# Optimization experiments

Hardware: AMD Instinct MI355X
Metric: run time of the kernel (lower is better)

## Reference

```python
import jax, jax.numpy as jnp
import numpy as np

HIGH_DENSITY = 1000.0
GRID = 128          # W = D = H
NUM_COLORS = 6
N_POINTS = 4194304  # ~2^22 query samples
EXPECTED_DENSITY_SCALE = 1.0
TEMPERATURE = 1.0
HALF_EXTENT = GRID / 2.0  # voxel_size 1.0, grid centered at origin -> AABB [-64, 64]


def trilinear_sample(vol, pts):
    """torch grid_sample(mode='bilinear', align_corners=False, padding='zeros') on a 3D grid.
    vol: [X, Y, Z, C]; pts: [N, 3] normalized (x, y, z) in [-1, 1]. Returns [N, C]."""
    X, Y, Z, C = vol.shape
    sizes = jnp.array([X, Y, Z], dtype=pts.dtype)
    pos = ((pts + 1.0) * sizes - 1.0) * 0.5  # align_corners=False unnormalize
    base = jnp.floor(pos)
    frac = pos - base                         # [N, 3]
    base = base.astype(jnp.int32)
    maxi = jnp.array([X - 1, Y - 1, Z - 1], dtype=jnp.int32)
    out = jnp.zeros((pts.shape[0], C), dtype=vol.dtype)
    for dx in (0, 1):
        for dy in (0, 1):
            for dz in (0, 1):
                off = jnp.array([dx, dy, dz], dtype=jnp.int32)
                idx = base + off
                valid = jnp.all((idx >= 0) & (idx <= maxi), axis=-1)  # zero padding
                ic = jnp.clip(idx, 0, maxi)
                v = vol[ic[:, 0], ic[:, 1], ic[:, 2]]                 # [N, C] gather
                offf = jnp.array([dx, dy, dz], dtype=pts.dtype)
                w = jnp.prod(jnp.where(offf == 1.0, frac, 1.0 - frac), axis=-1)
                out = out + v * (w * valid.astype(pts.dtype))[:, None]
    return out


def st_softmax(x, temperature):
    """Straight-through softmax: hard one-hot(argmax) forward, softmax(x*T) gradient."""
    soft = jax.nn.softmax(x * temperature, axis=-1)
    hard = jax.nn.one_hot(jnp.argmax(x, axis=-1), x.shape[-1], dtype=x.dtype)
    return soft + jax.lax.stop_gradient(hard - soft)


def setup_inputs() -> dict:
    key = jax.random.key(0)
    k1, k2, k3, k4 = jax.random.split(key, 4)
    points = jax.random.uniform(k1, (N_POINTS, 3), dtype=jnp.float32,
                                minval=-60.0, maxval=60.0)
    densities = jax.random.normal(k2, (GRID, GRID, GRID, 2), dtype=jnp.float32)
    features = jax.random.normal(k3, (GRID, GRID, GRID, NUM_COLORS), dtype=jnp.float32)
    palette = jax.random.uniform(k4, (NUM_COLORS, 3), dtype=jnp.float32)
    return {"points": points, "densities": densities, "features": features,
            "palette": palette}


def reference(points, densities, features, palette):
    # normalize world points from AABB to [-1, 1] (adjust_dynamic_range, slack=True)
    npts = points / HALF_EXTENT                           # [N, 3]
    # density pre-activation: abs(raw * expected_density_scale)
    dens_pre = jnp.abs(densities * EXPECTED_DENSITY_SCALE)  # [X, Y, Z, 2]
    d_interp = trilinear_sample(dens_pre, npts)           # [N, 2]
    f_interp = trilinear_sample(features, npts)           # [N, NUM_COLORS]
    # VA quantization: ST softmax over {empty, occupied} logits -> hard occupancy
    d_soft = st_softmax(d_interp, TEMPERATURE)            # [N, 2]
    density = d_soft[:, 1:2] * HIGH_DENSITY               # [N, 1]
    # ST softmax over palette weights -> hard palette color lookup
    f_soft = st_softmax(f_interp, TEMPERATURE)            # [N, NUM_COLORS]
    rgb = f_soft @ palette                                # [N, 3]
    return jnp.concatenate([density, rgb], axis=-1)       # [N, 4]
```

## Files before the change

### kernel.cpp

```cpp
#include <hip/hip_runtime.h>

static constexpr int G = 128;
static constexpr size_t NVOX = (size_t)G * G * G;
static constexpr size_t ENTRIES_PER_PAR = (size_t)64 * 64 * 64;
static constexpr size_t NENTRIES = 8 * ENTRIES_PER_PAR;
static constexpr size_t P_BYTES = NENTRIES * 64;
static constexpr size_t C_BYTES = NVOX * 8;
static constexpr size_t WS_TWOSTAGE = P_BYTES + C_BYTES;
static constexpr size_t WS_DIRECT   = P_BYTES;


__device__ __forceinline__ uint32_t quant8(float v) {
    float c = fminf(fmaxf(v, -4.0f), 4.0f);
    return (uint32_t)((c + 4.0f) * 31.875f + 0.5f);
}

__device__ __forceinline__ uint2 make_rec8(const float2* __restrict__ dens,
                                           const float* __restrict__ feat,
                                           int vox) {
    float2 d = dens[vox];
    float delta = fabsf(d.y) - fabsf(d.x);
    int code = (int)((delta + 8.0f) * 4095.9375f + 0.5f);
    code = code < 0 ? 0 : (code > 65535 ? 65535 : code);
    const float2* fp = (const float2*)(feat + (size_t)vox * 6);
    float2 a = fp[0], b = fp[1], c = fp[2];
    uint2 r;
    r.x = (uint32_t)code | (quant8(a.x) << 16) | (quant8(a.y) << 24);
    r.y = quant8(b.x) | (quant8(b.y) << 8) | (quant8(c.x) << 16) | (quant8(c.y) << 24);
    return r;
}

__global__ __launch_bounds__(256) void compress_voxels(const float2* __restrict__ dens,
                                                       const float* __restrict__ feat,
                                                       uint2* __restrict__ C) {
    size_t v = (size_t)blockIdx.x * blockDim.x + threadIdx.x;
    if (v >= NVOX) return;
    C[v] = make_rec8(dens, feat, (int)v);
}

__global__ __launch_bounds__(256) void build_blocks_compact(const uint2* __restrict__ C,
                                                            uint4* __restrict__ P4) {
    size_t t = (size_t)blockIdx.x * blockDim.x + threadIdx.x;
    if (t >= NENTRIES) return;
    int p = (int)(t >> 18);
    int e = (int)(t & (ENTRIES_PER_PAR - 1));
    int xb = e >> 12, yb = (e >> 6) & 63, zb = e & 63;
    int x0 = 2 * xb + ((p >> 2) & 1);
    int y0 = 2 * yb + ((p >> 1) & 1);
    int z0 = 2 * zb + (p & 1);

    uint2 r[8];
    #pragma unroll
    for (int s = 0; s < 8; ++s) {
        int x = x0 + ((s >> 2) & 1); x = x < G ? x : G - 1;
        int y = y0 + ((s >> 1) & 1); y = y < G ? y : G - 1;
        int z = z0 + (s & 1);        z = z < G ? z : G - 1;
        r[s] = C[(size_t)(x * G + y) * G + z];
    }
    size_t o = t * 4;
    P4[o + 0] = make_uint4(r[0].x, r[0].y, r[1].x, r[1].y);
    P4[o + 1] = make_uint4(r[2].x, r[2].y, r[3].x, r[3].y);
    P4[o + 2] = make_uint4(r[4].x, r[4].y, r[5].x, r[5].y);
    P4[o + 3] = make_uint4(r[6].x, r[6].y, r[7].x, r[7].y);
}

__global__ __launch_bounds__(256) void build_blocks_direct(const float2* __restrict__ dens,
                                                           const float* __restrict__ feat,
                                                           uint4* __restrict__ P4) {
    size_t t = (size_t)blockIdx.x * blockDim.x + threadIdx.x;
    if (t >= NENTRIES) return;
    int p = (int)(t >> 18);
    int e = (int)(t & (ENTRIES_PER_PAR - 1));
    int xb = e >> 12, yb = (e >> 6) & 63, zb = e & 63;
    int x0 = 2 * xb + ((p >> 2) & 1);
    int y0 = 2 * yb + ((p >> 1) & 1);
    int z0 = 2 * zb + (p & 1);

    uint2 r[8];
    #pragma unroll
    for (int s = 0; s < 8; ++s) {
        int x = x0 + ((s >> 2) & 1); x = x < G ? x : G - 1;
        int y = y0 + ((s >> 1) & 1); y = y < G ? y : G - 1;
        int z = z0 + (s & 1);        z = z < G ? z : G - 1;
        r[s] = make_rec8(dens, feat, (x * G + y) * G + z);
    }
    size_t o = t * 4;
    P4[o + 0] = make_uint4(r[0].x, r[0].y, r[1].x, r[1].y);
    P4[o + 1] = make_uint4(r[2].x, r[2].y, r[3].x, r[3].y);
    P4[o + 2] = make_uint4(r[4].x, r[4].y, r[5].x, r[5].y);
    P4[o + 3] = make_uint4(r[6].x, r[6].y, r[7].x, r[7].y);
}

__global__ __launch_bounds__(256) void voxel_main(
    const float* __restrict__ points,
    const uint4* __restrict__ P4,
    const float2* __restrict__ dens,
    const float* __restrict__ palette,
    float4* __restrict__ out, int n)
{
#pragma clang fp contract(off)
    int i = blockIdx.x * blockDim.x + threadIdx.x;
    if (i >= n) return;

    float px_ = points[3 * i + 0];
    float py_ = points[3 * i + 1];
    float pz_ = points[3 * i + 2];

    float posx = ((px_ / 64.0f + 1.0f) * 128.0f - 1.0f) * 0.5f;
    float posy = ((py_ / 64.0f + 1.0f) * 128.0f - 1.0f) * 0.5f;
    float posz = ((pz_ / 64.0f + 1.0f) * 128.0f - 1.0f) * 0.5f;

    float bx = floorf(posx), by = floorf(posy), bz = floorf(posz);
    int ix = (int)bx, iy = (int)by, iz = (int)bz;
    float fx = posx - bx, fy = posy - by, fz = posz - bz;

    float wx0 = 1.0f - fx, wx1 = fx;
    float wy0 = 1.0f - fy, wy1 = fy;
    float wz0 = 1.0f - fz, wz1 = fz;

    float w[8];
    w[0] = (wx0 * wy0) * wz0; w[1] = (wx0 * wy0) * wz1;
    w[2] = (wx0 * wy1) * wz0; w[3] = (wx0 * wy1) * wz1;
    w[4] = (wx1 * wy0) * wz0; w[5] = (wx1 * wy0) * wz1;
    w[6] = (wx1 * wy1) * wz0; w[7] = (wx1 * wy1) * wz1;

    int p = ((ix & 1) << 2) | ((iy & 1) << 1) | (iz & 1);
    int e = ((ix >> 1) << 12) | ((iy >> 1) << 6) | (iz >> 1);
    const uint4* L = P4 + (((size_t)p << 18) + (size_t)e) * 4;
    uint4 L0 = L[0], L1 = L[1], L2 = L[2], L3 = L[3];

    float S = 0.0f;
    float F0 = 0.f, F1 = 0.f, F2 = 0.f, F3 = 0.f, F4 = 0.f, F5 = 0.f;
    bool suspect = false;

    uint32_t wl[8] = {L0.x, L0.z, L1.x, L1.z, L2.x, L2.z, L3.x, L3.z};
    uint32_t wh[8] = {L0.y, L0.w, L1.y, L1.w, L2.y, L2.w, L3.y, L3.w};

    #pragma unroll
    for (int s = 0; s < 8; ++s) {
        uint32_t lo = wl[s], hi = wh[s];
        uint32_t code = lo & 0xffffu;
        suspect = suspect || (code == 0u) || (code == 65535u);
        float dl = (float)code * (16.0f / 65535.0f) - 8.0f;
        float ws = w[s];
        S  += dl * ws;
        F0 += (float)((lo >> 16) & 255u) * ws;
        F1 += (float)(lo >> 24) * ws;
        F2 += (float)(hi & 255u) * ws;
        F3 += (float)((hi >> 8) & 255u) * ws;
        F4 += (float)((hi >> 16) & 255u) * ws;
        F5 += (float)(hi >> 24) * ws;
    }

    float density;
    if (!suspect && fabsf(S) > 4e-4f) {
        density = (S > 0.0f) ? 1000.0f : 0.0f;
    } else {
        double D0 = 0.0, D1 = 0.0;
        #pragma unroll
        for (int s = 0; s < 8; ++s) {
            int idx = ((ix + ((s >> 2) & 1)) * G + (iy + ((s >> 1) & 1))) * G + (iz + (s & 1));
            float2 dv = dens[idx];
            D0 += fabs((double)dv.x) * (double)w[s];
            D1 += fabs((double)dv.y) * (double)w[s];
        }
        density = (D1 > D0) ? 1000.0f : 0.0f;
    }

    int k = 0;
    float m = F0;
    if (F1 > m) { m = F1; k = 1; }
    if (F2 > m) { m = F2; k = 2; }
    if (F3 > m) { m = F3; k = 3; }
    if (F4 > m) { m = F4; k = 4; }
    if (F5 > m) { m = F5; k = 5; }

    float4 o;
    o.x = density;
    o.y = palette[3 * k + 0];
    o.z = palette[3 * k + 1];
    o.w = palette[3 * k + 2];
    out[i] = o;
}

__global__ __launch_bounds__(256) void voxel_art_direct(
    const float* __restrict__ points,
    const float2* __restrict__ dens,
    const float* __restrict__ feat,
    const float* __restrict__ palette,
    float4* __restrict__ out, int n)
{
#pragma clang fp contract(off)
    int i = blockIdx.x * blockDim.x + threadIdx.x;
    if (i >= n) return;
    float px = points[3 * i], py = points[3 * i + 1], pz = points[3 * i + 2];
    float posx = ((px / 64.0f + 1.0f) * 128.0f - 1.0f) * 0.5f;
    float posy = ((py / 64.0f + 1.0f) * 128.0f - 1.0f) * 0.5f;
    float posz = ((pz / 64.0f + 1.0f) * 128.0f - 1.0f) * 0.5f;
    float bx = floorf(posx), by = floorf(posy), bz = floorf(posz);
    int ix = (int)bx, iy = (int)by, iz = (int)bz;
    float fx = posx - bx, fy = posy - by, fz = posz - bz;
    int basei = (ix * G + iy) * G + iz;
    float wx[2] = {1.0f - fx, fx}, wy[2] = {1.0f - fy, fy}, wz[2] = {1.0f - fz, fz};
    double d0 = 0.0, d1 = 0.0;
    float f0 = 0, f1 = 0, f2 = 0, f3 = 0, f4 = 0, f5 = 0;
    #pragma unroll
    for (int dx = 0; dx < 2; ++dx)
    #pragma unroll
    for (int dy = 0; dy < 2; ++dy)
    #pragma unroll
    for (int dz = 0; dz < 2; ++dz) {
        int idx = basei + dx * (G * G) + dy * G + dz;
        float wq = (wx[dx] * wy[dy]) * wz[dz];
        float2 dv = dens[idx];
        d0 += fabs((double)dv.x) * (double)wq;
        d1 += fabs((double)dv.y) * (double)wq;
        const float2* fp2 = (const float2*)(feat + (size_t)idx * 6);
        float2 a = fp2[0], b = fp2[1], c = fp2[2];
        f0 += a.x * wq; f1 += a.y * wq; f2 += b.x * wq;
        f3 += b.y * wq; f4 += c.x * wq; f5 += c.y * wq;
    }
    float density = (d1 > d0) ? 1000.0f : 0.0f;
    int k = 0; float m = f0;
    if (f1 > m) { m = f1; k = 1; }
    if (f2 > m) { m = f2; k = 2; }
    if (f3 > m) { m = f3; k = 3; }
    if (f4 > m) { m = f4; k = 4; }
    if (f5 > m) { m = f5; k = 5; }
    out[i] = make_float4(density, palette[3 * k], palette[3 * k + 1], palette[3 * k + 2]);
}

extern "C" void kernel_launch(void* const* d_in, const int* in_sizes, int n_in,
                              void* d_out, int out_size, void* d_ws, size_t ws_size,
                              hipStream_t stream) {
    const float*  points  = (const float*)d_in[0];
    const float2* dens    = (const float2*)d_in[1];
    const float*  feat    = (const float*)d_in[2];
    const float*  palette = (const float*)d_in[3];
    float4*       out     = (float4*)d_out;

    int n = in_sizes[0] / 3;
    int threads = 256;
    int blocks = (n + threads - 1) / threads;

    if (ws_size >= WS_TWOSTAGE) {
        uint4* P4 = (uint4*)d_ws;
        uint2* C  = (uint2*)((char*)d_ws + P_BYTES);
        compress_voxels<<<(int)((NVOX + 255) / 256), 256, 0, stream>>>(dens, feat, C);
        build_blocks_compact<<<(int)((NENTRIES + 255) / 256), 256, 0, stream>>>(C, P4);
        voxel_main<<<blocks, threads, 0, stream>>>(points, P4, dens, palette, out, n);
    } else if (ws_size >= WS_DIRECT) {
        uint4* P4 = (uint4*)d_ws;
        build_blocks_direct<<<(int)((NENTRIES + 255) / 256), 256, 0, stream>>>(dens, feat, P4);
        voxel_main<<<blocks, threads, 0, stream>>>(points, P4, dens, palette, out, n);
    } else {
        voxel_art_direct<<<blocks, threads, 0, stream>>>(points, dens, feat, palette, out, n);
    }
}
```

Before: 269.3 us.

## Build all parity blocks per entry from shared neighbourhood; process two points per thread

The block-building kernel now has each thread load a 3x3x3 neighbourhood of compressed voxels once and emit all eight parity-shifted 2x2x2 records, instead of one thread per parity re-reading eight voxels. The main lookup kernel handles two points per thread, loading coordinates with float2 loads and issuing both points' table gathers before the decode math to raise memory-level parallelism. This costs more registers per thread and fewer threads in flight.

```diff
diff --git a/kernel.cpp b/kernel.cpp
--- a/kernel.cpp
+++ b/kernel.cpp
@@ -38,30 +38,45 @@
     C[v] = make_rec8(dens, feat, (int)v);
 }
 
-__global__ __launch_bounds__(256) void build_blocks_compact(const uint2* __restrict__ C,
-                                                            uint4* __restrict__ P4) {
+__global__ __launch_bounds__(256) void build_blocks_v2(const uint2* __restrict__ C,
+                                                       uint4* __restrict__ P4) {
     size_t t = (size_t)blockIdx.x * blockDim.x + threadIdx.x;
-    if (t >= NENTRIES) return;
-    int p = (int)(t >> 18);
-    int e = (int)(t & (ENTRIES_PER_PAR - 1));
-    int xb = e >> 12, yb = (e >> 6) & 63, zb = e & 63;
-    int x0 = 2 * xb + ((p >> 2) & 1);
-    int y0 = 2 * yb + ((p >> 1) & 1);
-    int z0 = 2 * zb + (p & 1);
-
-    uint2 r[8];
-    #pragma unroll
-    for (int s = 0; s < 8; ++s) {
-        int x = x0 + ((s >> 2) & 1); x = x < G ? x : G - 1;
-        int y = y0 + ((s >> 1) & 1); y = y < G ? y : G - 1;
-        int z = z0 + (s & 1);        z = z < G ? z : G - 1;
-        r[s] = C[(size_t)(x * G + y) * G + z];
-    }
-    size_t o = t * 4;
-    P4[o + 0] = make_uint4(r[0].x, r[0].y, r[1].x, r[1].y);
-    P4[o + 1] = make_uint4(r[2].x, r[2].y, r[3].x, r[3].y);
-    P4[o + 2] = make_uint4(r[4].x, r[4].y, r[5].x, r[5].y);
-    P4[o + 3] = make_uint4(r[6].x, r[6].y, r[7].x, r[7].y);
+    if (t >= ENTRIES_PER_PAR) return;
+    int xb = (int)(t >> 12), yb = (int)((t >> 6) & 63), zb = (int)(t & 63);
+
+    int xs[3], ys[3], zs[3];
+    #pragma unroll
+    for (int d = 0; d < 3; ++d) {
+        int x = 2 * xb + d; xs[d] = x < G ? x : G - 1;
+        int y = 2 * yb + d; ys[d] = y < G ? y : G - 1;
+        int z = 2 * zb + d; zs[d] = z < G ? z : G - 1;
+    }
+
+    uint2 r[3][3][3];
+    #pragma unroll
+    for (int dx = 0; dx < 3; ++dx)
+        #pragma unroll
+        for (int dy = 0; dy < 3; ++dy) {
+            const uint2* row = C + (size_t)(xs[dx] * G + ys[dy]) * G;
+            #pragma unroll
+            for (int dz = 0; dz < 3; ++dz)
+                r[dx][dy][dz] = row[zs[dz]];
+        }
+
+    size_t e4 = t * 4;
+    #pragma unroll
+    for (int p = 0; p < 8; ++p) {
+        int px = (p >> 2) & 1, py = (p >> 1) & 1, pz = p & 1;
+        uint4* dst = P4 + ((size_t)p << 20) + e4;
+        uint2 s0 = r[px + 0][py + 0][pz + 0], s1 = r[px + 0][py + 0][pz + 1];
+        uint2 s2 = r[px + 0][py + 1][pz + 0], s3 = r[px + 0][py + 1][pz + 1];
+        uint2 s4 = r[px + 1][py + 0][pz + 0], s5 = r[px + 1][py + 0][pz + 1];
+        uint2 s6 = r[px + 1][py + 1][pz + 0], s7 = r[px + 1][py + 1][pz + 1];
+        dst[0] = make_uint4(s0.x, s0.y, s1.x, s1.y);
+        dst[1] = make_uint4(s2.x, s2.y, s3.x, s3.y);
+        dst[2] = make_uint4(s4.x, s4.y, s5.x, s5.y);
+        dst[3] = make_uint4(s6.x, s6.y, s7.x, s7.y);
+    }
 }
 
 __global__ __launch_bounds__(256) void build_blocks_direct(const float2* __restrict__ dens,
@@ -75,7 +90,6 @@
     int x0 = 2 * xb + ((p >> 2) & 1);
     int y0 = 2 * yb + ((p >> 1) & 1);
     int z0 = 2 * zb + (p & 1);
-
     uint2 r[8];
     #pragma unroll
     for (int s = 0; s < 8; ++s) {
@@ -91,7 +105,81 @@
     P4[o + 3] = make_uint4(r[6].x, r[6].y, r[7].x, r[7].y);
 }
 
-__global__ __launch_bounds__(256) void voxel_main(
+struct PtWork {
+    int ix, iy, iz;
+    float w[8];
+    const uint4* L;
+};
+
+__device__ __forceinline__ void pt_setup(float px_, float py_, float pz_,
+                                         const uint4* __restrict__ P4, PtWork& W) {
+    float posx = ((px_ / 64.0f + 1.0f) * 128.0f - 1.0f) * 0.5f;
+    float posy = ((py_ / 64.0f + 1.0f) * 128.0f - 1.0f) * 0.5f;
+    float posz = ((pz_ / 64.0f + 1.0f) * 128.0f - 1.0f) * 0.5f;
+    float bx = floorf(posx), by = floorf(posy), bz = floorf(posz);
+    W.ix = (int)bx; W.iy = (int)by; W.iz = (int)bz;
+    float fx = posx - bx, fy = posy - by, fz = posz - bz;
+    float wx0 = 1.0f - fx, wx1 = fx;
+    float wy0 = 1.0f - fy, wy1 = fy;
+    float wz0 = 1.0f - fz, wz1 = fz;
+    W.w[0] = (wx0 * wy0) * wz0; W.w[1] = (wx0 * wy0) * wz1;
+    W.w[2] = (wx0 * wy1) * wz0; W.w[3] = (wx0 * wy1) * wz1;
+    W.w[4] = (wx1 * wy0) * wz0; W.w[5] = (wx1 * wy0) * wz1;
+    W.w[6] = (wx1 * wy1) * wz0; W.w[7] = (wx1 * wy1) * wz1;
+    int p = ((W.ix & 1) << 2) | ((W.iy & 1) << 1) | (W.iz & 1);
+    int e = ((W.ix >> 1) << 12) | ((W.iy >> 1) << 6) | (W.iz >> 1);
+    W.L = P4 + (((size_t)p << 18) + (size_t)e) * 4;
+}
+
+__device__ __forceinline__ float4 pt_finish(const PtWork& W,
+                                            uint4 L0, uint4 L1, uint4 L2, uint4 L3,
+                                            const float2* __restrict__ dens,
+                                            const float* __restrict__ palette) {
+    float S = 0.0f;
+    float F0 = 0.f, F1 = 0.f, F2 = 0.f, F3 = 0.f, F4 = 0.f, F5 = 0.f;
+    bool suspect = false;
+    uint32_t wl[8] = {L0.x, L0.z, L1.x, L1.z, L2.x, L2.z, L3.x, L3.z};
+    uint32_t wh[8] = {L0.y, L0.w, L1.y, L1.w, L2.y, L2.w, L3.y, L3.w};
+    #pragma unroll
+    for (int s = 0; s < 8; ++s) {
+        uint32_t lo = wl[s], hi = wh[s];
+        uint32_t code = lo & 0xffffu;
+        suspect = suspect || (code == 0u) || (code == 65535u);
+        float dl = (float)code * (16.0f / 65535.0f) - 8.0f;
+        float ws = W.w[s];
+        S  += dl * ws;
+        F0 += (float)((lo >> 16) & 255u) * ws;
+        F1 += (float)(lo >> 24) * ws;
+        F2 += (float)(hi & 255u) * ws;
+        F3 += (float)((hi >> 8) & 255u) * ws;
+        F4 += (float)((hi >> 16) & 255u) * ws;
+        F5 += (float)(hi >> 24) * ws;
+    }
+    float density;
+    if (!suspect && fabsf(S) > 4e-4f) {
+        density = (S > 0.0f) ? 1000.0f : 0.0f;
+    } else {
+        double D0 = 0.0, D1 = 0.0;
+        #pragma unroll
+        for (int s = 0; s < 8; ++s) {
+            int idx = ((W.ix + ((s >> 2) & 1)) * G + (W.iy + ((s >> 1) & 1))) * G + (W.iz + (s & 1));
+            float2 dv = dens[idx];
+            D0 += fabs((double)dv.x) * (double)W.w[s];
+            D1 += fabs((double)dv.y) * (double)W.w[s];
+        }
+        density = (D1 > D0) ? 1000.0f : 0.0f;
+    }
+    int k = 0;
+    float m = F0;
+    if (F1 > m) { m = F1; k = 1; }
+    if (F2 > m) { m = F2; k = 2; }
+    if (F3 > m) { m = F3; k = 3; }
+    if (F4 > m) { m = F4; k = 4; }
+    if (F5 > m) { m = F5; k = 5; }
+    return make_float4(density, palette[3 * k], palette[3 * k + 1], palette[3 * k + 2]);
+}
+
+__global__ __launch_bounds__(256) void voxel_main2(
     const float* __restrict__ points,
     const uint4* __restrict__ P4,
     const float2* __restrict__ dens,
@@ -99,88 +187,26 @@
     float4* __restrict__ out, int n)
 {
 #pragma clang fp contract(off)
-    int i = blockIdx.x * blockDim.x + threadIdx.x;
-    if (i >= n) return;
-
-    float px_ = points[3 * i + 0];
-    float py_ = points[3 * i + 1];
-    float pz_ = points[3 * i + 2];
-
-    float posx = ((px_ / 64.0f + 1.0f) * 128.0f - 1.0f) * 0.5f;
-    float posy = ((py_ / 64.0f + 1.0f) * 128.0f - 1.0f) * 0.5f;
-    float posz = ((pz_ / 64.0f + 1.0f) * 128.0f - 1.0f) * 0.5f;
-
-    float bx = floorf(posx), by = floorf(posy), bz = floorf(posz);
-    int ix = (int)bx, iy = (int)by, iz = (int)bz;
-    float fx = posx - bx, fy = posy - by, fz = posz - bz;
-
-    float wx0 = 1.0f - fx, wx1 = fx;
-    float wy0 = 1.0f - fy, wy1 = fy;
-    float wz0 = 1.0f - fz, wz1 = fz;
-
-    float w[8];
-    w[0] = (wx0 * wy0) * wz0; w[1] = (wx0 * wy0) * wz1;
-    w[2] = (wx0 * wy1) * wz0; w[3] = (wx0 * wy1) * wz1;
-    w[4] = (wx1 * wy0) * wz0; w[5] = (wx1 * wy0) * wz1;
-    w[6] = (wx1 * wy1) * wz0; w[7] = (wx1 * wy1) * wz1;
-
-    int p = ((ix & 1) << 2) | ((iy & 1) << 1) | (iz & 1);
-    int e = ((ix >> 1) << 12) | ((iy >> 1) << 6) | (iz >> 1);
-    const uint4* L = P4 + (((size_t)p << 18) + (size_t)e) * 4;
-    uint4 L0 = L[0], L1 = L[1], L2 = L[2], L3 = L[3];
-
-    float S = 0.0f;
-    float F0 = 0.f, F1 = 0.f, F2 = 0.f, F3 = 0.f, F4 = 0.f, F5 = 0.f;
-    bool suspect = false;
-
-    uint32_t wl[8] = {L0.x, L0.z, L1.x, L1.z, L2.x, L2.z, L3.x, L3.z};
-    uint32_t wh[8] = {L0.y, L0.w, L1.y, L1.w, L2.y, L2.w, L3.y, L3.w};
-
-    #pragma unroll
-    for (int s = 0; s < 8; ++s) {
-        uint32_t lo = wl[s], hi = wh[s];
-        uint32_t code = lo & 0xffffu;
-        suspect = suspect || (code == 0u) || (code == 65535u);
-        float dl = (float)code * (16.0f / 65535.0f) - 8.0f;
-        float ws = w[s];
-        S  += dl * ws;
-        F0 += (float)((lo >> 16) & 255u) * ws;
-        F1 += (float)(lo >> 24) * ws;
-        F2 += (float)(hi & 255u) * ws;
-        F3 += (float)((hi >> 8) & 255u) * ws;
-        F4 += (float)((hi >> 16) & 255u) * ws;
-        F5 += (float)(hi >> 24) * ws;
-    }
-
-    float density;
-    if (!suspect && fabsf(S) > 4e-4f) {
-        density = (S > 0.0f) ? 1000.0f : 0.0f;
-    } else {
-        double D0 = 0.0, D1 = 0.0;
-        #pragma unroll
-        for (int s = 0; s < 8; ++s) {
-            int idx = ((ix + ((s >> 2) & 1)) * G + (iy + ((s >> 1) & 1))) * G + (iz + (s & 1));
-            float2 dv = dens[idx];
-            D0 += fabs((double)dv.x) * (double)w[s];
-            D1 += fabs((double)dv.y) * (double)w[s];
-        }
-        density = (D1 > D0) ? 1000.0f : 0.0f;
-    }
-
-    int k = 0;
-    float m = F0;
-    if (F1 > m) { m = F1; k = 1; }
-    if (F2 > m) { m = F2; k = 2; }
-    if (F3 > m) { m = F3; k = 3; }
-    if (F4 > m) { m = F4; k = 4; }
-    if (F5 > m) { m = F5; k = 5; }
-
-    float4 o;
-    o.x = density;
-    o.y = palette[3 * k + 0];
-    o.z = palette[3 * k + 1];
-    o.w = palette[3 * k + 2];
-    out[i] = o;
+    int t = blockIdx.x * blockDim.x + threadIdx.x;
+    int i0 = 2 * t;
+    if (i0 >= n) return;
+    bool two = (i0 + 1) < n;
+
+    const float2* pp = (const float2*)points;
+    float2 a = pp[3 * t + 0];
+    float2 b = pp[3 * t + 1];
+    float2 c = two ? pp[3 * t + 2] : make_float2(0.f, 0.f);
+
+    PtWork W0, W1;
+    pt_setup(a.x, a.y, b.x, P4, W0);
+    pt_setup(b.y, c.x, c.y, P4, W1);
+    if (!two) W1.L = W0.L;
+
+    uint4 A0 = W0.L[0], A1 = W0.L[1], A2 = W0.L[2], A3 = W0.L[3];
+    uint4 B0 = W1.L[0], B1 = W1.L[1], B2 = W1.L[2], B3 = W1.L[3];
+
+    out[i0] = pt_finish(W0, A0, A1, A2, A3, dens, palette);
+    if (two) out[i0 + 1] = pt_finish(W1, B0, B1, B2, B3, dens, palette);
 }
 
 __global__ __launch_bounds__(256) void voxel_art_direct(
@@ -216,9 +242,9 @@
         d0 += fabs((double)dv.x) * (double)wq;
         d1 += fabs((double)dv.y) * (double)wq;
         const float2* fp2 = (const float2*)(feat + (size_t)idx * 6);
-        float2 a = fp2[0], b = fp2[1], c = fp2[2];
-        f0 += a.x * wq; f1 += a.y * wq; f2 += b.x * wq;
-        f3 += b.y * wq; f4 += c.x * wq; f5 += c.y * wq;
+        float2 aa = fp2[0], bb = fp2[1], cc = fp2[2];
+        f0 += aa.x * wq; f1 += aa.y * wq; f2 += bb.x * wq;
+        f3 += bb.y * wq; f4 += cc.x * wq; f5 += cc.y * wq;
     }
     float density = (d1 > d0) ? 1000.0f : 0.0f;
     int k = 0; float m = f0;
@@ -241,19 +267,20 @@
 
     int n = in_sizes[0] / 3;
     int threads = 256;
-    int blocks = (n + threads - 1) / threads;
 
     if (ws_size >= WS_TWOSTAGE) {
         uint4* P4 = (uint4*)d_ws;
         uint2* C  = (uint2*)((char*)d_ws + P_BYTES);
         compress_voxels<<<(int)((NVOX + 255) / 256), 256, 0, stream>>>(dens, feat, C);
-        build_blocks_compact<<<(int)((NENTRIES + 255) / 256), 256, 0, stream>>>(C, P4);
-        voxel_main<<<blocks, threads, 0, stream>>>(points, P4, dens, palette, out, n);
+        build_blocks_v2<<<(int)((ENTRIES_PER_PAR + 255) / 256), 256, 0, stream>>>(C, P4);
+        int nt = (n + 1) / 2;
+        voxel_main2<<<(nt + threads - 1) / threads, threads, 0, stream>>>(points, P4, dens, palette, out, n);
     } else if (ws_size >= WS_DIRECT) {
         uint4* P4 = (uint4*)d_ws;
         build_blocks_direct<<<(int)((NENTRIES + 255) / 256), 256, 0, stream>>>(dens, feat, P4);
-        voxel_main<<<blocks, threads, 0, stream>>>(points, P4, dens, palette, out, n);
+        int nt = (n + 1) / 2;
+        voxel_main2<<<(nt + threads - 1) / threads, threads, 0, stream>>>(points, P4, dens, palette, out, n);
     } else {
-        voxel_art_direct<<<blocks, threads, 0, stream>>>(points, dens, feat, palette, out, n);
-    }
-}
+        voxel_art_direct<<<(n + threads - 1) / threads, threads, 0, stream>>>(points, dens, feat, palette, out, n);
+    }
+}
```

Result: slower. 282.0 us (+4.7%).
